# Kernel tuning notes

Measured on AMD Instinct MI355X. Metric: run time of the kernel, lower is better.

## Reference

```python
import jax, jax.numpy as jnp
import numpy as np

B, T, D, H = 4, 2048, 1024, 16
HD = D // H  # 64
EPS = 1e-5


def setup_inputs() -> dict:
    key = jax.random.key(0)
    ks = jax.random.split(key, 8)
    s = 0.02
    return {
        "X": jax.random.normal(ks[0], (B, T, D), dtype=jnp.float32),
        # per-head projection weights stacked: [H, D, HD] (no bias, matches nn.Linear(bias=False))
        "Wq": jax.random.normal(ks[1], (H, D, HD), dtype=jnp.float32) * s,
        "Wk": jax.random.normal(ks[2], (H, D, HD), dtype=jnp.float32) * s,
        "Wv": jax.random.normal(ks[3], (H, D, HD), dtype=jnp.float32) * s,
        "ln1_g": jnp.ones((D,), jnp.float32),
        "ln1_b": jnp.zeros((D,), jnp.float32),
        "W1": jax.random.normal(ks[4], (D, 4 * D), dtype=jnp.float32) * s,
        "b1": jnp.zeros((4 * D,), jnp.float32),
        "W2": jax.random.normal(ks[5], (4 * D, D), dtype=jnp.float32) * s,
        "b2": jnp.zeros((D,), jnp.float32),
        "ln2_g": jnp.ones((D,), jnp.float32),
        "ln2_b": jnp.zeros((D,), jnp.float32),
    }


def _layer_norm(x, g, b):
    m = jnp.mean(x, axis=-1, keepdims=True)
    v = jnp.mean((x - m) ** 2, axis=-1, keepdims=True)
    return (x - m) / jnp.sqrt(v + EPS) * g + b


def reference(X, Wq, Wk, Wv, ln1_g, ln1_b, W1, b1, W2, b2, ln2_g, ln2_b):
    # multi-head causal self-attention (naive full-matrix, matching source)
    Q = jnp.einsum('btd,hde->bhte', X, Wq)
    K = jnp.einsum('btd,hde->bhte', X, Wk)
    V = jnp.einsum('btd,hde->bhte', X, Wv)
    scores = jnp.einsum('bhte,bhse->bhts', Q, K) / jnp.sqrt(jnp.float32(HD))
    causal = jnp.tril(jnp.ones((T, T), dtype=bool))
    scores = jnp.where(causal, scores, jnp.finfo(scores.dtype).min)
    attn = jax.nn.softmax(scores, axis=-1)
    Yh = jnp.einsum('bhts,bhse->bhte', attn, V)  # [B,H,T,HD]
    Y = jnp.transpose(Yh, (0, 2, 1, 3)).reshape(B, T, D)  # concat heads

    X1 = _layer_norm(Y + X, ln1_g, ln1_b)
    ff = jax.nn.relu(X1 @ W1 + b1) @ W2 + b2  # dropout inactive (eval)
    X2 = ff + X1
    return _layer_norm(X2, ln2_g, ln2_b)
```

## Files before the change

kernel.cpp:

```cpp
#include <hip/hip_runtime.h>
#include <cstdint>


typedef _Float16 f16x8 __attribute__((ext_vector_type(8)));
typedef _Float16 f16x4 __attribute__((ext_vector_type(4)));
typedef float    f32x4 __attribute__((ext_vector_type(4)));

#define DEVI __device__ __forceinline__

typedef __attribute__((address_space(1))) uint32_t gas1_u32;
typedef __attribute__((address_space(3))) uint32_t las3_u32;

DEVI void gl2lds16(const void* g, void* l) {
  __builtin_amdgcn_global_load_lds((gas1_u32*)(uintptr_t)g,
                                   (las3_u32*)(uintptr_t)l, 16, 0, 0);
}

__global__ __launch_bounds__(256) void cvt_f32_f16(const float* __restrict__ src,
                                                   _Float16* __restrict__ dst, int n) {
  int i = (blockIdx.x * 256 + threadIdx.x) * 8;
  if (i >= n) return;
  float4 a = *(const float4*)&src[i];
  float4 b = *(const float4*)&src[i + 4];
  f16x8 o;
  o[0] = (_Float16)a.x; o[1] = (_Float16)a.y; o[2] = (_Float16)a.z; o[3] = (_Float16)a.w;
  o[4] = (_Float16)b.x; o[5] = (_Float16)b.y; o[6] = (_Float16)b.z; o[7] = (_Float16)b.w;
  *(f16x8*)&dst[i] = o;
}

__global__ __launch_bounds__(256) void transpose_f2h(
    const float* __restrict__ src, int srcSliceStride,
    _Float16* __restrict__ dst, int dstRow0, int dstSliceRows,
    int K, int N, int dstK, float scale) {
  __shared__ _Float16 T[64 * 72];
  const int k0 = blockIdx.x * 64;
  const int n0 = blockIdx.y * 64;
  src += (size_t)blockIdx.z * srcSliceStride;
  const int rowbase = dstRow0 + blockIdx.z * dstSliceRows + n0;
  const int tid = threadIdx.x;
#pragma unroll
  for (int p = 0; p < 4; ++p) {
    int c = p * 256 + tid;
    int kl = c >> 4;
    int nl = (c & 15) * 4;
    float4 v = *(const float4*)&src[(size_t)(k0 + kl) * N + n0 + nl];
    T[(nl + 0) * 72 + kl] = (_Float16)(v.x * scale);
    T[(nl + 1) * 72 + kl] = (_Float16)(v.y * scale);
    T[(nl + 2) * 72 + kl] = (_Float16)(v.z * scale);
    T[(nl + 3) * 72 + kl] = (_Float16)(v.w * scale);
  }
  __syncthreads();
#pragma unroll
  for (int p = 0; p < 2; ++p) {
    int c = p * 256 + tid;
    int nl = c >> 3;
    int kc = (c & 7) * 8;
    f16x8 vv = *(const f16x8*)&T[nl * 72 + kc];
    *(f16x8*)&dst[(size_t)(rowbase + nl) * dstK + k0 + kc] = vv;
  }
}

__global__ __launch_bounds__(256) void transpose_v(
    const _Float16* __restrict__ Vh, _Float16* __restrict__ Vt) {
  __shared__ _Float16 T[64 * 72];
  const int t0 = blockIdx.x * 64;
  const size_t hb = (size_t)blockIdx.y * (2048 * 64);
  const int tid = threadIdx.x;
#pragma unroll
  for (int it = 0; it < 2; ++it) {
    const int c = it * 256 + tid;
    const int tl = c >> 3;
    const int ec = (c & 7) * 8;
    *(f16x8*)&T[tl * 72 + ec] =
        *(const f16x8*)&Vh[hb + (size_t)(t0 + tl) * 64 + ec];
  }
  __syncthreads();
#pragma unroll
  for (int it = 0; it < 2; ++it) {
    const int c = it * 256 + tid;
    const int el = c >> 3;
    const int tc = (c & 7) * 8;
    f16x8 o;
#pragma unroll
    for (int jj = 0; jj < 8; ++jj) o[jj] = T[(tc + jj) * 72 + el];
    *(f16x8*)&Vt[hb + (size_t)el * 2048 + t0 + tc] = o;
  }
}

template <int NF, int MODE>
__global__ __launch_bounds__(512, 1) void gemm8(
    const _Float16* __restrict__ A, const _Float16* __restrict__ Bt,
    int K, int N,
    const float* __restrict__ bias, const _Float16* __restrict__ residH,
    float* __restrict__ outF, _Float16* __restrict__ outH,
    _Float16* __restrict__ outQ, _Float16* __restrict__ outKp,
    _Float16* __restrict__ outV) {
  constexpr int BN = NF * 64;
  constexpr int NBH = BN / 128;
  __shared__ _Float16 As[2][2][128 * 64];
  __shared__ _Float16 Bs[2][NBH][128 * 64];
  const int tid = threadIdx.x;
  const int lane = tid & 63;
  const int w = tid >> 6;
  const int wr = w >> 2, wc = w & 3;
  const int lr = lane & 15, g = lane >> 4;
  const int m0 = blockIdx.y * 256, n0 = blockIdx.x * BN;
  const int NT = K >> 6;

  const _Float16* Ab = A + (size_t)m0 * K;
  const _Float16* Bb = Bt + (size_t)n0 * K;

  f32x4 acc[8][NF] = {};

  auto STG = [&](const _Float16* src, _Float16* dst) {
#pragma unroll
    for (int it = 0; it < 2; ++it) {
      const int c = it * 512 + tid;
      const int r = c >> 3;
      const int ts = (c & 7) ^ (r & 7);
      gl2lds16(src + (size_t)r * K + ts * 8, dst + c * 8);
    }
  };

  STG(Ab, &As[0][0][0]);
  STG(Ab + 128 * (size_t)K, &As[0][1][0]);
  STG(Bb, &Bs[0][0][0]);
  if constexpr (NBH == 2) STG(Bb + 128 * (size_t)K, &Bs[0][NBH - 1][0]);
  STG(Ab + 64, &As[1][0][0]);
  STG(Ab + 128 * (size_t)K + 64, &As[1][1][0]);
  STG(Bb + 64, &Bs[1][0][0]);
  asm volatile("s_waitcnt vmcnt(6)" ::: "memory");
  __builtin_amdgcn_sched_barrier(0xF);
  __builtin_amdgcn_s_barrier();
  __builtin_amdgcn_sched_barrier(0xF);

  f16x8 afA[4][2], afB[4][2], bfL[NF / 2][2], bfH[NF / 2][2];

#define LDA_(af, MLO, buf)                                                   \
  _Pragma("unroll") for (int mf = 0; mf < 4; ++mf) {                         \
    const int rl = (MLO + mf) * 16 + lr;                                     \
    _Pragma("unroll") for (int k2 = 0; k2 < 2; ++k2)                         \
      af[mf][k2] = *(const f16x8*)&As[buf][wr][rl * 64 +                     \
                      (((k2 * 4 + g) ^ (rl & 7)) << 3)];                     \
  }
#define LDB_(bf, NLO, buf)                                                   \
  _Pragma("unroll") for (int nf = 0; nf < NF / 2; ++nf) {                    \
    const int rb = wc * (BN / 4) + (NLO + nf) * 16 + lr;                     \
    _Pragma("unroll") for (int k2 = 0; k2 < 2; ++k2)                         \
      bf[nf][k2] = *(const f16x8*)&Bs[buf][rb >> 7][(rb & 127) * 64 +        \
                      (((k2 * 4 + g) ^ (rb & 7)) << 3)];                     \
  }
#define MMA_(af, bf, MB, NB)                                                 \
  __builtin_amdgcn_s_setprio(1);                                             \
  _Pragma("unroll") for (int mf = 0; mf < 4; ++mf)                           \
  _Pragma("unroll") for (int nf = 0; nf < NF / 2; ++nf)                      \
  _Pragma("unroll") for (int k2 = 0; k2 < 2; ++k2)                           \
    acc[(MB) + mf][(NB) + nf] = __builtin_amdgcn_mfma_f32_16x16x32_f16(      \
        af[mf][k2], bf[nf][k2], acc[(MB) + mf][(NB) + nf], 0, 0, 0);         \
  __builtin_amdgcn_s_setprio(0);
#define PHASE_END                                                            \
  __builtin_amdgcn_sched_barrier(0xF);                                       \
  __builtin_amdgcn_s_barrier();                                              \
  __builtin_amdgcn_sched_barrier(0xF);

  for (int t = 0; t < NT; ++t) {
    const int cur = t & 1, nxt = cur ^ 1;
    LDA_(afA, 0, cur);
    LDB_(bfL, 0, cur);
    if (NBH == 2 && t + 1 < NT)
      STG(Bb + 128 * (size_t)K + (size_t)(t + 1) * 64, &Bs[nxt][NBH - 1][0]);
    PHASE_END;
    MMA_(afA, bfL, 0, 0);
    PHASE_END;
    LDA_(afB, 4, cur);
    PHASE_END;
    MMA_(afB, bfL, 4, 0);
    PHASE_END;
    LDB_(bfH, NF / 2, cur);
    if (t + 2 < NT) STG(Ab + (size_t)(t + 2) * 64, &As[cur][0][0]);
    PHASE_END;
    MMA_(afA, bfH, 0, NF / 2);
    PHASE_END;
    if (t + 2 < NT) {
      STG(Ab + 128 * (size_t)K + (size_t)(t + 2) * 64, &As[cur][1][0]);
      STG(Bb + (size_t)(t + 2) * 64, &Bs[cur][0][0]);
    }
    if (t == NT - 2) {
      asm volatile("s_waitcnt vmcnt(0)" ::: "memory");
    } else if (t < NT - 2) {
      asm volatile("s_waitcnt vmcnt(6)" ::: "memory");
    }
    PHASE_END;
    MMA_(afB, bfH, 4, NF / 2);
    PHASE_END;
  }
#undef LDA_
#undef LDB_
#undef MMA_
#undef PHASE_END

#pragma unroll
  for (int mf = 0; mf < 8; ++mf) {
#pragma unroll
    for (int nf = 0; nf < NF; ++nf) {
#pragma unroll
      for (int rr = 0; rr < 4; ++rr) {
        const int row = m0 + wr * 128 + mf * 16 + g * 4 + rr;
        const int col = n0 + wc * (BN / 4) + nf * 16 + lr;
        float v = acc[mf][nf][rr];
        if constexpr (MODE == 0) {
          const int qkv = col >> 10;
          const int h = (col >> 6) & 15;
          const int e = col & 63;
          const int b = row >> 11;
          const int tt = row & 2047;
          const size_t idx = (((size_t)b * 16 + h) * 2048 + tt) * 64 + e;
          const _Float16 hv = (_Float16)v;
          if (qkv == 0)      outQ[idx] = hv;
          else if (qkv == 1) outKp[idx] = hv;
          else               outV[idx] = hv;
        } else if constexpr (MODE == 1) {
          float o = fmaxf(v + bias[col], 0.0f);
          outH[(size_t)row * N + col] = (_Float16)o;
        } else {
          outF[(size_t)row * N + col] =
              v + bias[col] + (float)residH[(size_t)row * N + col];
        }
      }
    }
  }
}

__global__ __launch_bounds__(256, 2) void attn_fwd4(
    const _Float16* __restrict__ Qg, const _Float16* __restrict__ Kg,
    const _Float16* __restrict__ Vtg, float* __restrict__ Yg) {
  __shared__ _Float16 Ksm[2][64 * 64];
  __shared__ _Float16 Vts[2][64 * 64];
  __shared__ _Float16 Psm[128 * 72];
  const int tid = threadIdx.x;
  const int lane = tid & 63;
  const int w = tid >> 6;
  const int lr = lane & 15, g = lane >> 4;

  const int bid = blockIdx.x;
  const int bh  = (bid & 7) * 8 + ((bid >> 3) & 7);
  const int p   = bid >> 6;
  const int qtA = p, qtB = 15 - p;
  const int njA = 2 * p + 2;
  const int ntot = 34;

  const size_t hbo = (size_t)bh * (2048 * 64);
  const _Float16* Qb = Qg + hbo;
  const _Float16* Kb = Kg + hbo;
  const _Float16* Vb = Vtg + hbo;
  float* Yb = Yg + hbo;

  f16x8 qfA[2][2], qfB[2][2];
#pragma unroll
  for (int mi = 0; mi < 2; ++mi) {
    const int rA = qtA * 128 + mi * 64 + w * 16 + lr;
    const int rB = qtB * 128 + mi * 64 + w * 16 + lr;
#pragma unroll
    for (int ss = 0; ss < 2; ++ss) {
      qfA[mi][ss] = *(const f16x8*)&Qb[(size_t)rA * 64 + ss * 32 + g * 8];
      qfB[mi][ss] = *(const f16x8*)&Qb[(size_t)rB * 64 + ss * 32 + g * 8];
    }
  }

  float mA[2][4], mB[2][4];
  f32x4 accYA[2][4] = {}, accYB[2][4] = {};
  f32x4 accLA[2] = {}, accLB[2] = {};
#pragma unroll
  for (int mi = 0; mi < 2; ++mi)
#pragma unroll
    for (int r = 0; r < 4; ++r) { mA[mi][r] = -3.0e38f; mB[mi][r] = -3.0e38f; }

  f16x8 ones;
#pragma unroll
  for (int i = 0; i < 8; ++i) ones[i] = (_Float16)1.0f;

  auto STAGE = [&](int bufi, int tk0) {
#pragma unroll
    for (int it = 0; it < 2; ++it) {
      const int c = it * 256 + tid;
      const int r = c >> 3;
      const int ts = (c & 7) ^ (r & 7);
      gl2lds16(Kb + (size_t)(tk0 + r) * 64 + ts * 8, &Ksm[bufi][c * 8]);
      gl2lds16(Vb + (size_t)r * 2048 + tk0 + ts * 8, &Vts[bufi][c * 8]);
    }
  };

  auto BODY = [&](int bufi, int qbase, int tk0, const f16x8 (&qf)[2][2],
                  float (&m_run)[2][4], f32x4 (&accY)[2][4], f32x4 (&accL)[2]) {
    const _Float16* Ks = Ksm[bufi];
    const _Float16* Vs = Vts[bufi];
#pragma unroll
    for (int mi = 0; mi < 2; ++mi) {
      const int qlo = qbase + mi * 64 + w * 16;
      if (tk0 > qlo + 15) continue;
      f32x4 s[4] = {};
      __builtin_amdgcn_s_setprio(1);
#pragma unroll
      for (int ni = 0; ni < 4; ++ni) {
        const int row = ni * 16 + lr;
#pragma unroll
        for (int kk = 0; kk < 2; ++kk) {
          const int ts = (kk * 4 + g) ^ (row & 7);
          const f16x8 kf = *(const f16x8*)&Ks[row * 64 + ts * 8];
          s[ni] = __builtin_amdgcn_mfma_f32_16x16x32_f16(qf[mi][kk], kf, s[ni], 0, 0, 0);
        }
      }
      __builtin_amdgcn_s_setprio(0);
      if (tk0 + 63 > qlo) {
#pragma unroll
        for (int ni = 0; ni < 4; ++ni)
#pragma unroll
          for (int r = 0; r < 4; ++r) {
            const int qa = qlo + g * 4 + r;
            const int ka = tk0 + ni * 16 + lr;
            if (ka > qa) s[ni][r] = -3.0e38f;
          }
      }
      float lm[4];
      bool need = false;
#pragma unroll
      for (int r = 0; r < 4; ++r) {
        lm[r] = fmaxf(fmaxf(s[0][r], s[1][r]), fmaxf(s[2][r], s[3][r]));
        need = need || (lm[r] > m_run[mi][r] + 10.0f);
      }
      if (__any(need)) {
#pragma unroll
        for (int r = 0; r < 4; ++r) {
          float pm = lm[r];
          pm = fmaxf(pm, __shfl_xor(pm, 1));
          pm = fmaxf(pm, __shfl_xor(pm, 2));
          pm = fmaxf(pm, __shfl_xor(pm, 4));
          pm = fmaxf(pm, __shfl_xor(pm, 8));
          if (pm > m_run[mi][r]) {
            const float sc = exp2f(m_run[mi][r] - pm);
            m_run[mi][r] = pm;
            accL[mi][r] *= sc;
#pragma unroll
            for (int ne = 0; ne < 4; ++ne) accY[mi][ne][r] *= sc;
          }
        }
      }
#pragma unroll
      for (int ni = 0; ni < 4; ++ni)
#pragma unroll
        for (int r = 0; r < 4; ++r) {
          const float pv = exp2f(s[ni][r] - m_run[mi][r]);
          Psm[(mi * 64 + w * 16 + g * 4 + r) * 72 + ni * 16 + lr] = (_Float16)pv;
        }
      const int prow = mi * 64 + w * 16 + lr;
      __builtin_amdgcn_s_setprio(1);
#pragma unroll
      for (int ss = 0; ss < 2; ++ss) {
        const f16x8 pa = *(const f16x8*)&Psm[prow * 72 + ss * 32 + g * 8];
        accL[mi] = __builtin_amdgcn_mfma_f32_16x16x32_f16(pa, ones, accL[mi], 0, 0, 0);
#pragma unroll
        for (int ne = 0; ne < 4; ++ne) {
          const int vrow = ne * 16 + lr;
          const int tsv = (ss * 4 + g) ^ (vrow & 7);
          const f16x8 vbf = *(const f16x8*)&Vs[vrow * 64 + tsv * 8];
          accY[mi][ne] = __builtin_amdgcn_mfma_f32_16x16x32_f16(pa, vbf, accY[mi][ne], 0, 0, 0);
        }
      }
      __builtin_amdgcn_s_setprio(0);
    }
  };

  STAGE(0, 0);
  for (int u = 0; u < ntot; ++u) {
    asm volatile("s_waitcnt vmcnt(0)" ::: "memory");
    __builtin_amdgcn_s_barrier();
    __builtin_amdgcn_sched_barrier(0xF);
    const int cur = u & 1;
    if (u + 1 < ntot) {
      const int un = u + 1;
      STAGE(cur ^ 1, (un < njA ? un : un - njA) * 64);
    }
    if (u < njA) BODY(cur, qtA * 128, u * 64, qfA, mA, accYA, accLA);
    else         BODY(cur, qtB * 128, (u - njA) * 64, qfB, mB, accYB, accLB);
  }

#pragma unroll
  for (int mi = 0; mi < 2; ++mi)
#pragma unroll
    for (int r = 0; r < 4; ++r) {
      const float invA = 1.0f / accLA[mi][r];
      const float invB = 1.0f / accLB[mi][r];
      const int qaA = qtA * 128 + mi * 64 + w * 16 + g * 4 + r;
      const int qaB = qtB * 128 + mi * 64 + w * 16 + g * 4 + r;
#pragma unroll
      for (int ne = 0; ne < 4; ++ne) {
        Yb[(size_t)qaA * 64 + ne * 16 + lr] = accYA[mi][ne][r] * invA;
        Yb[(size_t)qaB * 64 + ne * 16 + lr] = accYB[mi][ne][r] * invB;
      }
    }
}

__global__ __launch_bounds__(256) void ln1_fused(
    const float* __restrict__ Yf, const float* __restrict__ X,
    const float* __restrict__ gam, const float* __restrict__ bet,
    _Float16* __restrict__ X1h) {
  const int row = blockIdx.x;
  const int b = row >> 11, t = row & 2047;
  const int tid = threadIdx.x;
  const int d0 = tid * 4;
  const int h = d0 >> 6, e = d0 & 63;
  const float4 y = *(const float4*)&Yf[(((size_t)b * 16 + h) * 2048 + t) * 64 + e];
  const float4 x = *(const float4*)&X[(size_t)row * 1024 + d0];
  float v0 = y.x + x.x, v1 = y.y + x.y, v2 = y.z + x.z, v3 = y.w + x.w;
  float s = v0 + v1 + v2 + v3;
  float q = v0 * v0 + v1 * v1 + v2 * v2 + v3 * v3;
  for (int off = 32; off; off >>= 1) { s += __shfl_xor(s, off); q += __shfl_xor(q, off); }
  __shared__ float red[8];
  const int w = tid >> 6;
  if ((tid & 63) == 0) { red[w] = s; red[4 + w] = q; }
  __syncthreads();
  s = red[0] + red[1] + red[2] + red[3];
  q = red[4] + red[5] + red[6] + red[7];
  const float mean = s * (1.f / 1024.f);
  const float rstd = rsqrtf(q * (1.f / 1024.f) - mean * mean + 1e-5f);
  const float4 G = *(const float4*)&gam[d0];
  const float4 Bv = *(const float4*)&bet[d0];
  f16x4 oh;
  oh[0] = (_Float16)((v0 - mean) * rstd * G.x + Bv.x);
  oh[1] = (_Float16)((v1 - mean) * rstd * G.y + Bv.y);
  oh[2] = (_Float16)((v2 - mean) * rstd * G.z + Bv.z);
  oh[3] = (_Float16)((v3 - mean) * rstd * G.w + Bv.w);
  *(f16x4*)&X1h[(size_t)row * 1024 + d0] = oh;
}

__global__ __launch_bounds__(256) void ln2_kernel(
    const float* __restrict__ In, const float* __restrict__ gam,
    const float* __restrict__ bet, float* __restrict__ Out) {
  const int row = blockIdx.x;
  const int tid = threadIdx.x;
  const int d0 = tid * 4;
  const float4 v4 = *(const float4*)&In[(size_t)row * 1024 + d0];
  float v0 = v4.x, v1 = v4.y, v2 = v4.z, v3 = v4.w;
  float s = v0 + v1 + v2 + v3;
  float q = v0 * v0 + v1 * v1 + v2 * v2 + v3 * v3;
  for (int off = 32; off; off >>= 1) { s += __shfl_xor(s, off); q += __shfl_xor(q, off); }
  __shared__ float red[8];
  const int w = tid >> 6;
  if ((tid & 63) == 0) { red[w] = s; red[4 + w] = q; }
  __syncthreads();
  s = red[0] + red[1] + red[2] + red[3];
  q = red[4] + red[5] + red[6] + red[7];
  const float mean = s * (1.f / 1024.f);
  const float rstd = rsqrtf(q * (1.f / 1024.f) - mean * mean + 1e-5f);
  const float4 G = *(const float4*)&gam[d0];
  const float4 Bv = *(const float4*)&bet[d0];
  float4 o;
  o.x = (v0 - mean) * rstd * G.x + Bv.x;
  o.y = (v1 - mean) * rstd * G.y + Bv.y;
  o.z = (v2 - mean) * rstd * G.z + Bv.z;
  o.w = (v3 - mean) * rstd * G.w + Bv.w;
  *(float4*)&Out[(size_t)row * 1024 + d0] = o;
}

extern "C" void kernel_launch(void* const* d_in, const int* in_sizes, int n_in,
                              void* d_out, int out_size, void* d_ws, size_t ws_size,
                              hipStream_t stream) {
  (void)in_sizes; (void)n_in; (void)out_size; (void)ws_size;
  const float* X    = (const float*)d_in[0];
  const float* Wq   = (const float*)d_in[1];
  const float* Wk   = (const float*)d_in[2];
  const float* Wv   = (const float*)d_in[3];
  const float* ln1g = (const float*)d_in[4];
  const float* ln1b = (const float*)d_in[5];
  const float* W1   = (const float*)d_in[6];
  const float* b1   = (const float*)d_in[7];
  const float* W2   = (const float*)d_in[8];
  const float* b2   = (const float*)d_in[9];
  const float* ln2g = (const float*)d_in[10];
  const float* ln2b = (const float*)d_in[11];
  float* out = (float*)d_out;

  char* ws = (char*)d_ws;
  _Float16* Xh   = (_Float16*)(ws);
  _Float16* Vt   = (_Float16*)(ws);
  _Float16* Qh   = (_Float16*)(ws + 16777216ull);
  _Float16* Kh   = (_Float16*)(ws + 33554432ull);
  _Float16* Vh   = (_Float16*)(ws + 50331648ull);
  _Float16* ff1  = (_Float16*)(ws);
  _Float16* Wqkv = (_Float16*)(ws + 67108864ull);
  _Float16* W1t  = (_Float16*)(ws + 73400320ull);
  _Float16* W2t  = (_Float16*)(ws + 81788928ull);
  float*    Yf   = (float*)(ws + 90177536ull);
  _Float16* X1h  = (_Float16*)(ws + 157286400ull);

  cvt_f32_f16<<<dim3(4096), dim3(256), 0, stream>>>(X, Xh, 8388608);
  transpose_f2h<<<dim3(16, 1, 16), dim3(256), 0, stream>>>(Wq, 65536, Wqkv, 0,    64, 1024, 64, 1024, 0.18033688011112042f);
  transpose_f2h<<<dim3(16, 1, 16), dim3(256), 0, stream>>>(Wk, 65536, Wqkv, 1024, 64, 1024, 64, 1024, 1.0f);
  transpose_f2h<<<dim3(16, 1, 16), dim3(256), 0, stream>>>(Wv, 65536, Wqkv, 2048, 64, 1024, 64, 1024, 1.0f);
  transpose_f2h<<<dim3(16, 64, 1), dim3(256), 0, stream>>>(W1, 0, W1t, 0, 0, 1024, 4096, 1024, 1.0f);
  transpose_f2h<<<dim3(64, 16, 1), dim3(256), 0, stream>>>(W2, 0, W2t, 0, 0, 4096, 1024, 4096, 1.0f);

  gemm8<2, 0><<<dim3(24, 32), dim3(512), 0, stream>>>(
      Xh, Wqkv, 1024, 3072, nullptr, nullptr, nullptr, nullptr, Qh, Kh, Vh);

  transpose_v<<<dim3(32, 64), dim3(256), 0, stream>>>(Vh, Vt);

  attn_fwd4<<<dim3(512), dim3(256), 0, stream>>>(Qh, Kh, Vt, Yf);

  ln1_fused<<<dim3(8192), dim3(256), 0, stream>>>(Yf, X, ln1g, ln1b, X1h);

  gemm8<4, 1><<<dim3(16, 32), dim3(512), 0, stream>>>(
      X1h, W1t, 1024, 4096, b1, nullptr, nullptr, ff1, nullptr, nullptr, nullptr);

  gemm8<2, 2><<<dim3(8, 32), dim3(512), 0, stream>>>(
      ff1, W2t, 4096, 1024, b2, X1h, Yf, nullptr, nullptr, nullptr, nullptr);

  ln2_kernel<<<dim3(8192), dim3(256), 0, stream>>>(Yf, ln2g, ln2b, out);
}
```

Measured before the change: 386.4 us.

## Split GEMMs into 256x128 and 256x256 variants with XCD-aware block remap

Replaces the templated gemm8 with two kernels. gemm4 uses a 256x128 tile with 8 waves in a 4x2 layout for the QKV and FFN2 GEMMs. gemm8_ffn1 is a specialised 256x256 kernel for FFN1. All three GEMMs now use a 1D grid whose block index is remapped so consecutive blocks on the same XCD share rows, which should improve L2 reuse. FFN2 also writes its residual sum as fp16 instead of fp32, and ln2 reads fp16, cutting memory traffic at some cost in precision.

```diff
diff --git a/kernel.cpp b/kernel.cpp
--- a/kernel.cpp
+++ b/kernel.cpp
@@ -15,6 +15,11 @@
   __builtin_amdgcn_global_load_lds((gas1_u32*)(uintptr_t)g,
                                    (las3_u32*)(uintptr_t)l, 16, 0, 0);
 }
+
+#define FENCE_BAR                                                            \
+  __builtin_amdgcn_sched_barrier(0xF);                                       \
+  __builtin_amdgcn_s_barrier();                                              \
+  __builtin_amdgcn_sched_barrier(0xF);
 
 __global__ __launch_bounds__(256) void cvt_f32_f16(const float* __restrict__ src,
                                                    _Float16* __restrict__ dst, int n) {
@@ -87,30 +92,160 @@
   }
 }
 
-template <int NF, int MODE>
-__global__ __launch_bounds__(512, 1) void gemm8(
+template <int MODE>
+__global__ __launch_bounds__(512, 1) void gemm4(
     const _Float16* __restrict__ A, const _Float16* __restrict__ Bt,
-    int K, int N,
+    int K, int N, int nbx, int cpx,
     const float* __restrict__ bias, const _Float16* __restrict__ residH,
-    float* __restrict__ outF, _Float16* __restrict__ outH,
+    _Float16* __restrict__ outH,
     _Float16* __restrict__ outQ, _Float16* __restrict__ outKp,
     _Float16* __restrict__ outV) {
-  constexpr int BN = NF * 64;
-  constexpr int NBH = BN / 128;
   __shared__ _Float16 As[2][2][128 * 64];
-  __shared__ _Float16 Bs[2][NBH][128 * 64];
+  __shared__ _Float16 Bs[2][128 * 64];
+  const int tid = threadIdx.x;
+  const int lane = tid & 63;
+  const int w = tid >> 6;
+  const int wr = w >> 1, wc = w & 1;
+  const int lr = lane & 15, g = lane >> 4;
+  const int o = (blockIdx.x & 7) * cpx + (blockIdx.x >> 3);
+  const int m0 = (o / nbx) * 256, n0 = (o % nbx) * 128;
+  const int NT = K >> 6;
+
+  const _Float16* Ab = A + (size_t)m0 * K;
+  const _Float16* Bb = Bt + (size_t)n0 * K;
+
+  f32x4 acc[4][4] = {};
+
+  auto STG = [&](const _Float16* src, _Float16* dst) {
+#pragma unroll
+    for (int it = 0; it < 2; ++it) {
+      const int c = it * 512 + tid;
+      const int r = c >> 3;
+      const int ts = (c & 7) ^ (r & 7);
+      gl2lds16(src + (size_t)r * K + ts * 8, dst + c * 8);
+    }
+  };
+
+  STG(Ab, &As[0][0][0]);
+  STG(Ab + 128 * (size_t)K, &As[0][1][0]);
+  STG(Bb, &Bs[0][0]);
+  STG(Ab + 64, &As[1][0][0]);
+  STG(Ab + 128 * (size_t)K + 64, &As[1][1][0]);
+  STG(Bb + 64, &Bs[1][0]);
+  asm volatile("s_waitcnt vmcnt(6)" ::: "memory");
+  FENCE_BAR;
+
+  f16x8 af[4][2], bfL[2][2], bfH[2][2];
+
+  for (int t = 0; t < NT; ++t) {
+    const int b = t & 1;
+#pragma unroll
+    for (int mf = 0; mf < 4; ++mf) {
+      const int rl = (wr & 1) * 64 + mf * 16 + lr;
+#pragma unroll
+      for (int k2 = 0; k2 < 2; ++k2)
+        af[mf][k2] = *(const f16x8*)&As[b][wr >> 1]
+            [rl * 64 + (((k2 * 4 + g) ^ (rl & 7)) << 3)];
+    }
+#pragma unroll
+    for (int nf = 0; nf < 2; ++nf) {
+      const int rb = wc * 64 + nf * 16 + lr;
+#pragma unroll
+      for (int k2 = 0; k2 < 2; ++k2)
+        bfL[nf][k2] = *(const f16x8*)&Bs[b]
+            [rb * 64 + (((k2 * 4 + g) ^ (rb & 7)) << 3)];
+    }
+    FENCE_BAR;
+    if (t + 2 < NT) {
+      STG(Ab + (size_t)(t + 2) * 64, &As[b][0][0]);
+      STG(Ab + 128 * (size_t)K + (size_t)(t + 2) * 64, &As[b][1][0]);
+    }
+#pragma unroll
+    for (int nf = 0; nf < 2; ++nf) {
+      const int rb = wc * 64 + (nf + 2) * 16 + lr;
+#pragma unroll
+      for (int k2 = 0; k2 < 2; ++k2)
+        bfH[nf][k2] = *(const f16x8*)&Bs[b]
+            [rb * 64 + (((k2 * 4 + g) ^ (rb & 7)) << 3)];
+    }
+    __builtin_amdgcn_s_setprio(1);
+#pragma unroll
+    for (int mf = 0; mf < 4; ++mf)
+#pragma unroll
+      for (int nf = 0; nf < 2; ++nf)
+#pragma unroll
+        for (int k2 = 0; k2 < 2; ++k2)
+          acc[mf][nf] = __builtin_amdgcn_mfma_f32_16x16x32_f16(
+              af[mf][k2], bfL[nf][k2], acc[mf][nf], 0, 0, 0);
+    __builtin_amdgcn_s_setprio(0);
+    FENCE_BAR;
+    if (t + 2 < NT) STG(Bb + (size_t)(t + 2) * 64, &Bs[b][0]);
+    __builtin_amdgcn_s_setprio(1);
+#pragma unroll
+    for (int mf = 0; mf < 4; ++mf)
+#pragma unroll
+      for (int nf = 0; nf < 2; ++nf)
+#pragma unroll
+        for (int k2 = 0; k2 < 2; ++k2)
+          acc[mf][nf + 2] = __builtin_amdgcn_mfma_f32_16x16x32_f16(
+              af[mf][k2], bfH[nf][k2], acc[mf][nf + 2], 0, 0, 0);
+    __builtin_amdgcn_s_setprio(0);
+    if (t == NT - 2) {
+      asm volatile("s_waitcnt vmcnt(0)" ::: "memory");
+    } else if (t < NT - 2) {
+      asm volatile("s_waitcnt vmcnt(6)" ::: "memory");
+    }
+    FENCE_BAR;
+  }
+
+#pragma unroll
+  for (int mf = 0; mf < 4; ++mf) {
+#pragma unroll
+    for (int nf = 0; nf < 4; ++nf) {
+#pragma unroll
+      for (int rr = 0; rr < 4; ++rr) {
+        const int row = m0 + wr * 64 + mf * 16 + g * 4 + rr;
+        const int col = n0 + wc * 64 + nf * 16 + lr;
+        float v = acc[mf][nf][rr];
+        if constexpr (MODE == 0) {
+          const int qkv = col >> 10;
+          const int h = (col >> 6) & 15;
+          const int e = col & 63;
+          const int bb = row >> 11;
+          const int tt = row & 2047;
+          const size_t idx = (((size_t)bb * 16 + h) * 2048 + tt) * 64 + e;
+          const _Float16 hv = (_Float16)v;
+          if (qkv == 0)      outQ[idx] = hv;
+          else if (qkv == 1) outKp[idx] = hv;
+          else               outV[idx] = hv;
+        } else {
+          outH[(size_t)row * N + col] = (_Float16)(
+              v + bias[col] + (float)residH[(size_t)row * N + col]);
+        }
+      }
+    }
+  }
+}
+
+__global__ __launch_bounds__(512, 1) void gemm8_ffn1(
+    const _Float16* __restrict__ A, const _Float16* __restrict__ Bt,
+    int K, int N, int nbx, int cpx,
+    const float* __restrict__ bias, _Float16* __restrict__ outH) {
+  __shared__ _Float16 As[2][2][128 * 64];
+  __shared__ _Float16 Bs[2][2][128 * 64];
   const int tid = threadIdx.x;
   const int lane = tid & 63;
   const int w = tid >> 6;
   const int wr = w >> 2, wc = w & 3;
   const int lr = lane & 15, g = lane >> 4;
-  const int m0 = blockIdx.y * 256, n0 = blockIdx.x * BN;
+  const int o = (blockIdx.x & 7) * cpx + (blockIdx.x >> 3);
+  const int m0 = (o / nbx) * 256, n0 = (o % nbx) * 256;
   const int NT = K >> 6;
 
   const _Float16* Ab = A + (size_t)m0 * K;
   const _Float16* Bb = Bt + (size_t)n0 * K;
 
-  f32x4 acc[8][NF] = {};
+  f32x4 acc[8][4] = {};
 
   auto STG = [&](const _Float16* src, _Float16* dst) {
 #pragma unroll
@@ -125,62 +260,56 @@
   STG(Ab, &As[0][0][0]);
   STG(Ab + 128 * (size_t)K, &As[0][1][0]);
   STG(Bb, &Bs[0][0][0]);
-  if constexpr (NBH == 2) STG(Bb + 128 * (size_t)K, &Bs[0][NBH - 1][0]);
+  STG(Bb + 128 * (size_t)K, &Bs[0][1][0]);
   STG(Ab + 64, &As[1][0][0]);
   STG(Ab + 128 * (size_t)K + 64, &As[1][1][0]);
   STG(Bb + 64, &Bs[1][0][0]);
   asm volatile("s_waitcnt vmcnt(6)" ::: "memory");
-  __builtin_amdgcn_sched_barrier(0xF);
-  __builtin_amdgcn_s_barrier();
-  __builtin_amdgcn_sched_barrier(0xF);
-
-  f16x8 afA[4][2], afB[4][2], bfL[NF / 2][2], bfH[NF / 2][2];
-
-#define LDA_(af, MLO, buf)                                                   \
+  FENCE_BAR;
+
+  f16x8 afA[4][2], afB[4][2], bfL[2][2], bfH[2][2];
+
+#define LDA8_(af, MLO, buf)                                                  \
   _Pragma("unroll") for (int mf = 0; mf < 4; ++mf) {                         \
     const int rl = (MLO + mf) * 16 + lr;                                     \
     _Pragma("unroll") for (int k2 = 0; k2 < 2; ++k2)                         \
       af[mf][k2] = *(const f16x8*)&As[buf][wr][rl * 64 +                     \
                       (((k2 * 4 + g) ^ (rl & 7)) << 3)];                     \
   }
-#define LDB_(bf, NLO, buf)                                                   \
-  _Pragma("unroll") for (int nf = 0; nf < NF / 2; ++nf) {                    \
-    const int rb = wc * (BN / 4) + (NLO + nf) * 16 + lr;                     \
+#define LDB8_(bf, NLO, buf)                                                  \
+  _Pragma("unroll") for (int nf = 0; nf < 2; ++nf) {                         \
+    const int rb = wc * 64 + (NLO + nf) * 16 + lr;                           \
     _Pragma("unroll") for (int k2 = 0; k2 < 2; ++k2)                         \
       bf[nf][k2] = *(const f16x8*)&Bs[buf][rb >> 7][(rb & 127) * 64 +        \
                       (((k2 * 4 + g) ^ (rb & 7)) << 3)];                     \
   }
-#define MMA_(af, bf, MB, NB)                                                 \
+#define MMA8_(af, bf, MB, NB)                                                \
   __builtin_amdgcn_s_setprio(1);                                             \
   _Pragma("unroll") for (int mf = 0; mf < 4; ++mf)                           \
-  _Pragma("unroll") for (int nf = 0; nf < NF / 2; ++nf)                      \
+  _Pragma("unroll") for (int nf = 0; nf < 2; ++nf)                           \
   _Pragma("unroll") for (int k2 = 0; k2 < 2; ++k2)                           \
     acc[(MB) + mf][(NB) + nf] = __builtin_amdgcn_mfma_f32_16x16x32_f16(      \
         af[mf][k2], bf[nf][k2], acc[(MB) + mf][(NB) + nf], 0, 0, 0);         \
   __builtin_amdgcn_s_setprio(0);
-#define PHASE_END                                                            \
-  __builtin_amdgcn_sched_barrier(0xF);                                       \
-  __builtin_amdgcn_s_barrier();                                              \
-  __builtin_amdgcn_sched_barrier(0xF);
 
   for (int t = 0; t < NT; ++t) {
     const int cur = t & 1, nxt = cur ^ 1;
-    LDA_(afA, 0, cur);
-    LDB_(bfL, 0, cur);
-    if (NBH == 2 && t + 1 < NT)
-      STG(Bb + 128 * (size_t)K + (size_t)(t + 1) * 64, &Bs[nxt][NBH - 1][0]);
-    PHASE_END;
-    MMA_(afA, bfL, 0, 0);
-    PHASE_END;
-    LDA_(afB, 4, cur);
-    PHASE_END;
-    MMA_(afB, bfL, 4, 0);
-    PHASE_END;
-    LDB_(bfH, NF / 2, cur);
+    LDA8_(afA, 0, cur);
+    LDB8_(bfL, 0, cur);
+    if (t + 1 < NT)
+      STG(Bb + 128 * (size_t)K + (size_t)(t + 1) * 64, &Bs[nxt][1][0]);
+    FENCE_BAR;
+    MMA8_(afA, bfL, 0, 0);
+    FENCE_BAR;
+    LDA8_(afB, 4, cur);
+    FENCE_BAR;
+    MMA8_(afB, bfL, 4, 0);
+    FENCE_BAR;
+    LDB8_(bfH, 2, cur);
     if (t + 2 < NT) STG(Ab + (size_t)(t + 2) * 64, &As[cur][0][0]);
-    PHASE_END;
-    MMA_(afA, bfH, 0, NF / 2);
-    PHASE_END;
+    FENCE_BAR;
+    MMA8_(afA, bfH, 0, 2);
+    FENCE_BAR;
     if (t + 2 < NT) {
       STG(Ab + 128 * (size_t)K + (size_t)(t + 2) * 64, &As[cur][1][0]);
       STG(Bb + (size_t)(t + 2) * 64, &Bs[cur][0][0]);
@@ -190,42 +319,24 @@
     } else if (t < NT - 2) {
       asm volatile("s_waitcnt vmcnt(6)" ::: "memory");
     }
-    PHASE_END;
-    MMA_(afB, bfH, 4, NF / 2);
-    PHASE_END;
-  }
-#undef LDA_
-#undef LDB_
-#undef MMA_
-#undef PHASE_END
+    FENCE_BAR;
+    MMA8_(afB, bfH, 4, 2);
+    FENCE_BAR;
+  }
+#undef LDA8_
+#undef LDB8_
+#undef MMA8_
 
 #pragma unroll
   for (int mf = 0; mf < 8; ++mf) {
 #pragma unroll
-    for (int nf = 0; nf < NF; ++nf) {
+    for (int nf = 0; nf < 4; ++nf) {
 #pragma unroll
       for (int rr = 0; rr < 4; ++rr) {
         const int row = m0 + wr * 128 + mf * 16 + g * 4 + rr;
-        const int col = n0 + wc * (BN / 4) + nf * 16 + lr;
-        float v = acc[mf][nf][rr];
-        if constexpr (MODE == 0) {
-          const int qkv = col >> 10;
-          const int h = (col >> 6) & 15;
-          const int e = col & 63;
-          const int b = row >> 11;
-          const int tt = row & 2047;
-          const size_t idx = (((size_t)b * 16 + h) * 2048 + tt) * 64 + e;
-          const _Float16 hv = (_Float16)v;
-          if (qkv == 0)      outQ[idx] = hv;
-          else if (qkv == 1) outKp[idx] = hv;
-          else               outV[idx] = hv;
-        } else if constexpr (MODE == 1) {
-          float o = fmaxf(v + bias[col], 0.0f);
-          outH[(size_t)row * N + col] = (_Float16)o;
-        } else {
-          outF[(size_t)row * N + col] =
-              v + bias[col] + (float)residH[(size_t)row * N + col];
-        }
+        const int col = n0 + wc * 64 + nf * 16 + lr;
+        float v = fmaxf(acc[mf][nf][rr] + bias[col], 0.0f);
+        outH[(size_t)row * N + col] = (_Float16)v;
       }
     }
   }
@@ -434,13 +545,13 @@
 }
 
 __global__ __launch_bounds__(256) void ln2_kernel(
-    const float* __restrict__ In, const float* __restrict__ gam,
+    const _Float16* __restrict__ In, const float* __restrict__ gam,
     const float* __restrict__ bet, float* __restrict__ Out) {
   const int row = blockIdx.x;
   const int tid = threadIdx.x;
   const int d0 = tid * 4;
-  const float4 v4 = *(const float4*)&In[(size_t)row * 1024 + d0];
-  float v0 = v4.x, v1 = v4.y, v2 = v4.z, v3 = v4.w;
+  const f16x4 v4 = *(const f16x4*)&In[(size_t)row * 1024 + d0];
+  float v0 = (float)v4[0], v1 = (float)v4[1], v2 = (float)v4[2], v3 = (float)v4[3];
   float s = v0 + v1 + v2 + v3;
   float q = v0 * v0 + v1 * v1 + v2 * v2 + v3 * v3;
   for (int off = 32; off; off >>= 1) { s += __shfl_xor(s, off); q += __shfl_xor(q, off); }
@@ -491,6 +602,7 @@
   _Float16* W1t  = (_Float16*)(ws + 73400320ull);
   _Float16* W2t  = (_Float16*)(ws + 81788928ull);
   float*    Yf   = (float*)(ws + 90177536ull);
+  _Float16* X2h  = (_Float16*)(ws + 90177536ull);
   _Float16* X1h  = (_Float16*)(ws + 157286400ull);
 
   cvt_f32_f16<<<dim3(4096), dim3(256), 0, stream>>>(X, Xh, 8388608);
@@ -500,8 +612,8 @@
   transpose_f2h<<<dim3(16, 64, 1), dim3(256), 0, stream>>>(W1, 0, W1t, 0, 0, 1024, 4096, 1024, 1.0f);
   transpose_f2h<<<dim3(64, 16, 1), dim3(256), 0, stream>>>(W2, 0, W2t, 0, 0, 4096, 1024, 4096, 1.0f);
 
-  gemm8<2, 0><<<dim3(24, 32), dim3(512), 0, stream>>>(
-      Xh, Wqkv, 1024, 3072, nullptr, nullptr, nullptr, nullptr, Qh, Kh, Vh);
+  gemm4<0><<<dim3(768), dim3(512), 0, stream>>>(
+      Xh, Wqkv, 1024, 3072, 24, 96, nullptr, nullptr, nullptr, Qh, Kh, Vh);
 
   transpose_v<<<dim3(32, 64), dim3(256), 0, stream>>>(Vh, Vt);
 
@@ -509,11 +621,11 @@
 
   ln1_fused<<<dim3(8192), dim3(256), 0, stream>>>(Yf, X, ln1g, ln1b, X1h);
 
-  gemm8<4, 1><<<dim3(16, 32), dim3(512), 0, stream>>>(
-      X1h, W1t, 1024, 4096, b1, nullptr, nullptr, ff1, nullptr, nullptr, nullptr);
-
-  gemm8<2, 2><<<dim3(8, 32), dim3(512), 0, stream>>>(
-      ff1, W2t, 4096, 1024, b2, X1h, Yf, nullptr, nullptr, nullptr, nullptr);
-
-  ln2_kernel<<<dim3(8192), dim3(256), 0, stream>>>(Yf, ln2g, ln2b, out);
-}
+  gemm8_ffn1<<<dim3(512), dim3(512), 0, stream>>>(
+      X1h, W1t, 1024, 4096, 16, 64, b1, ff1);
+
+  gemm4<2><<<dim3(256), dim3(512), 0, stream>>>(
+      ff1, W2t, 4096, 1024, 8, 32, b2, X1h, X2h, nullptr, nullptr, nullptr);
+
+  ln2_kernel<<<dim3(8192), dim3(256), 0, stream>>>(X2h, ln2g, ln2b, out);
+}
```

Result: faster. 374.7 us (-3.0%).
